# Optimization experiments

Hardware: AMD Instinct MI355X
Metric: run time of the kernel (lower is better)

The kernel has to match this reference:

```python
import jax, jax.numpy as jnp
import numpy as np

D_MODEL = 256
N_HEADS = 8
N_LEVELS = 4
N_POINTS = 4
D_FFN = 1024
DH = D_MODEL // N_HEADS
SPATIAL = [(100, 100), (50, 50), (25, 25), (13, 13)]  # (H_l, W_l) per level


def setup_inputs() -> dict:
    key = jax.random.key(0)
    ks = iter(jax.random.split(key, 40))
    N, Lq = 8, 900
    Lin = sum(h * w for h, w in SPATIAL)
    p = lambda shape: jax.random.normal(next(ks), shape, jnp.float32) * 0.02
    inp = {
        'idx': 0,
        'tgt': jax.random.normal(next(ks), (N, Lq, D_MODEL), jnp.float32),
        'query_pos': jax.random.normal(next(ks), (N, Lq, D_MODEL), jnp.float32),
        'reference_points_def': jax.random.uniform(next(ks), (N, Lq, N_LEVELS, 2), jnp.float32),
        'src': jax.random.normal(next(ks), (N, Lin, D_MODEL), jnp.float32),
        'src_spatial_shapes': jnp.array(SPATIAL, jnp.int32),
        'level_start_index': jnp.array(np.cumsum([0] + [h * w for h, w in SPATIAL])[:-1], jnp.int32),
        'src_padding_mask': jnp.zeros((N, Lin), bool),
        # self-attn params
        'wq': p((D_MODEL, D_MODEL)), 'bq': jnp.zeros((D_MODEL,)),
        'wk': p((D_MODEL, D_MODEL)), 'bk': jnp.zeros((D_MODEL,)),
        'wv': p((D_MODEL, D_MODEL)), 'bv': jnp.zeros((D_MODEL,)),
        'wo': p((D_MODEL, D_MODEL)), 'bo': jnp.zeros((D_MODEL,)),
        # MSDeformAttn params
        'w_val': p((D_MODEL, D_MODEL)), 'b_val': jnp.zeros((D_MODEL,)),
        'w_off': p((D_MODEL, N_HEADS * N_LEVELS * N_POINTS * 2)), 'b_off': p((N_HEADS * N_LEVELS * N_POINTS * 2,)),
        'w_att': p((D_MODEL, N_HEADS * N_LEVELS * N_POINTS)), 'b_att': jnp.zeros((N_HEADS * N_LEVELS * N_POINTS,)),
        'w_out': p((D_MODEL, D_MODEL)), 'b_out': jnp.zeros((D_MODEL,)),
        # layer norms
        'ln1_g': jnp.ones((D_MODEL,)), 'ln1_b': jnp.zeros((D_MODEL,)),
        'ln2_g': jnp.ones((D_MODEL,)), 'ln2_b': jnp.zeros((D_MODEL,)),
        'ln3_g': jnp.ones((D_MODEL,)), 'ln3_b': jnp.zeros((D_MODEL,)),
        # FFN
        'w1': p((D_MODEL, D_FFN)), 'b1': jnp.zeros((D_FFN,)),
        'w2': p((D_FFN, D_MODEL)), 'b2': jnp.zeros((D_MODEL,)),
    }
    return inp


def _ln(x, g, b):
    m = x.mean(-1, keepdims=True)
    v = jnp.var(x, axis=-1, keepdims=True)
    return (x - m) / jnp.sqrt(v + 1e-5) * g + b


def _mha(q, k, v, wq, bq, wk, bk, wv, bv, wo, bo):
    N, Lq, _ = q.shape
    split = lambda x: x.reshape(N, -1, N_HEADS, DH).transpose(0, 2, 1, 3)  # (N,H,L,dh)
    qh = split(q @ wq + bq) * (1.0 / np.sqrt(DH))
    kh = split(k @ wk + bk)
    vh = split(v @ wv + bv)
    attn = jax.nn.softmax(jnp.einsum('bhqd,bhkd->bhqk', qh, kh), axis=-1)
    o = jnp.einsum('bhqk,bhkd->bhqd', attn, vh).transpose(0, 2, 1, 3).reshape(N, Lq, D_MODEL)
    return o @ wo + bo


def _bilinear(vflat, Hl, Wl, loc):
    # vflat: (N, H, Hl*Wl, dh); loc: (N, Lq, H, P, 2) normalized (x, y) in [0,1]
    N, Lq, _, P, _ = loc.shape
    x = loc[..., 0] * Wl - 0.5  # align_corners=False pixel coords
    y = loc[..., 1] * Hl - 0.5
    x0 = jnp.floor(x); y0 = jnp.floor(y)
    fx = (x - x0).transpose(0, 2, 1, 3).reshape(N, N_HEADS, Lq * P, 1)
    fy = (y - y0).transpose(0, 2, 1, 3).reshape(N, N_HEADS, Lq * P, 1)
    x0i = x0.astype(jnp.int32); y0i = y0.astype(jnp.int32)

    def gather(xi, yi):
        valid = ((xi >= 0) & (xi < Wl) & (yi >= 0) & (yi < Hl)).astype(vflat.dtype)
        idx = jnp.clip(yi, 0, Hl - 1) * Wl + jnp.clip(xi, 0, Wl - 1)
        idx = idx.transpose(0, 2, 1, 3).reshape(N, N_HEADS, Lq * P)
        g = jnp.take_along_axis(vflat, idx[..., None], axis=2)  # (N,H,Lq*P,dh)
        return g * valid.transpose(0, 2, 1, 3).reshape(N, N_HEADS, Lq * P, 1)

    v = (gather(x0i, y0i) * (1 - fx) * (1 - fy)
         + gather(x0i + 1, y0i) * fx * (1 - fy)
         + gather(x0i, y0i + 1) * (1 - fx) * fy
         + gather(x0i + 1, y0i + 1) * fx * fy)
    return v.reshape(N, N_HEADS, Lq, P, DH)


def _msdeform(query, ref, src, ss, pad_mask, w_val, b_val, w_off, b_off, w_att, b_att, w_out, b_out):
    N, Lq, _ = query.shape
    value = src @ w_val + b_val
    value = jnp.where(pad_mask[..., None], 0.0, value)  # masked_fill on padded memory
    off = (query @ w_off + b_off).reshape(N, Lq, N_HEADS, N_LEVELS, N_POINTS, 2)
    att = jax.nn.softmax((query @ w_att + b_att).reshape(N, Lq, N_HEADS, N_LEVELS * N_POINTS), axis=-1)
    att = att.reshape(N, Lq, N_HEADS, N_LEVELS, N_POINTS)
    normalizer = jnp.array([[w, h] for h, w in ss], jnp.float32)  # (L, 2) as (W_l, H_l)
    loc = ref[:, :, None, :, None, :] + off / normalizer[None, None, None, :, None, :]
    out = jnp.zeros((N, N_HEADS, Lq, DH), value.dtype)
    start = 0
    for l, (Hl, Wl) in enumerate(ss):
        vflat = value[:, start:start + Hl * Wl].reshape(N, Hl * Wl, N_HEADS, DH).transpose(0, 2, 1, 3)
        samp = _bilinear(vflat, Hl, Wl, loc[:, :, :, l])  # (N,H,Lq,P,dh)
        w_l = att[:, :, :, l].transpose(0, 2, 1, 3)  # (N,H,Lq,P)
        out = out + (samp * w_l[..., None]).sum(3)
        start += Hl * Wl
    out = out.transpose(0, 2, 1, 3).reshape(N, Lq, D_MODEL)
    return out @ w_out + b_out, loc


def reference(idx, tgt, query_pos, reference_points_def, src, src_spatial_shapes, level_start_index,
              src_padding_mask, wq, bq, wk, bk, wv, bv, wo, bo,
              w_val, b_val, w_off, b_off, w_att, b_att, w_out, b_out,
              ln1_g, ln1_b, ln2_g, ln2_b, ln3_g, ln3_b, w1, b1, w2, b2):
    ss = [tuple(int(v) for v in row) for row in np.asarray(src_spatial_shapes)]
    # self-attention (is_contrastive=False path)
    q = tgt + query_pos
    tgt2 = _mha(q, q, tgt, wq, bq, wk, bk, wv, bv, wo, bo)
    tgt = _ln(tgt + tgt2, ln2_g, ln2_b)
    # multiscale deformable cross-attention
    tgt2, _ = _msdeform(tgt + query_pos, reference_points_def, src, ss, src_padding_mask,
                        w_val, b_val, w_off, b_off, w_att, b_att, w_out, b_out)
    tgt = _ln(tgt + tgt2, ln1_g, ln1_b)
    # FFN
    tgt2 = jax.nn.relu(tgt @ w1 + b1) @ w2 + b2
    tgt = _ln(tgt + tgt2, ln3_g, ln3_b)
    return tgt
```

## Files before the change

kernel.cpp:

```cpp
#include <hip/hip_runtime.h>
#include <math.h>

#define NB 8
#define LQ 900
#define DM 256
#define NH 8
#define DH 32
#define NL 4
#define NP 4
#define DFFN 1024
#define LIN 13294
#define NVAL (NB*LIN)
#define MROW (NB*LQ)

typedef __attribute__((ext_vector_type(8))) short bf16x8;
typedef __attribute__((ext_vector_type(4))) float f32x4;

__device__ __forceinline__ unsigned short f2bf(float x) {
  unsigned u = __float_as_uint(x);
  u += 0x7FFFu + ((u >> 16) & 1u);
  return (unsigned short)(u >> 16);
}

__global__ __launch_bounds__(256) void pack_w(const float* __restrict__ Win,
                                              unsigned short* __restrict__ Wp) {
  const int idx = blockIdx.x * 256 + threadIdx.x;
  const int e = idx & 7;
  const int cs = (idx >> 3) & 3;
  const int n = (idx >> 5) & 255;
  const int kt = idx >> 13;
  const int c = cs ^ ((n >> 1) & 3);
  const int k = kt * 32 + c * 8 + e;
  Wp[idx] = f2bf(Win[(size_t)k * 256 + n]);
}

__global__ __launch_bounds__(256) void value_gemm2(const float* __restrict__ A,
                                                   const unsigned short* __restrict__ Wp,
                                                   const float* __restrict__ bias,
                                                   unsigned short* __restrict__ C,
                                                   int M) {
  __shared__ char lds[17408];
  short* As = (short*)lds;
  short* Bs = (short*)(lds + 4096);
  const int tid = threadIdx.x;
  const int lane = tid & 63, w = tid >> 6;
  const int wr = w >> 1, wc = w & 1;
  const int l15 = lane & 15, lc = lane >> 4;
  const int nwg = gridDim.x;
  const int qq = nwg >> 3, rr = nwg & 7;
  const int xcd = blockIdx.x & 7, pos = blockIdx.x >> 3;
  const int wgid = (xcd < rr ? xcd * (qq + 1) : rr * (qq + 1) + (xcd - rr) * qq) + pos;
  const int m0 = (wgid >> 1) * 64, n0 = (wgid & 1) * 128;
  const int ar = tid >> 2, ac = tid & 3;
  f32x4 acc[2][4] = {};
  for (int kt = 0; kt < 8; kt++) {
    const int arow = min(m0 + ar, M - 1);
    const float* ap = A + (size_t)arow * 256 + kt * 32 + ac * 8;
    const float4 a0 = ((const float4*)ap)[0], a1 = ((const float4*)ap)[1];
    const unsigned short* bp = Wp + ((size_t)(kt * 256 + n0)) * 32 + tid * 16;
    const uint4 b0 = ((const uint4*)bp)[0], b1 = ((const uint4*)bp)[1];
    __syncthreads();
    {
      bf16x8 av;
      av[0] = (short)f2bf(a0.x); av[1] = (short)f2bf(a0.y);
      av[2] = (short)f2bf(a0.z); av[3] = (short)f2bf(a0.w);
      av[4] = (short)f2bf(a1.x); av[5] = (short)f2bf(a1.y);
      av[6] = (short)f2bf(a1.z); av[7] = (short)f2bf(a1.w);
      *(bf16x8*)&As[ar * 32 + ((ac ^ ((ar >> 1) & 3)) << 3)] = av;
      *(uint4*)&Bs[tid * 16] = b0;
      *(uint4*)&Bs[tid * 16 + 8] = b1;
    }
    __syncthreads();
    bf16x8 af[2], bq[4];
#pragma unroll
    for (int i = 0; i < 2; i++) {
      const int row = wr * 32 + i * 16 + l15;
      af[i] = *(const bf16x8*)&As[row * 32 + ((lc ^ ((row >> 1) & 3)) << 3)];
    }
#pragma unroll
    for (int q = 0; q < 4; q++) {
      const int col = wc * 64 + q * 16 + l15;
      bq[q] = *(const bf16x8*)&Bs[col * 32 + ((lc ^ ((col >> 1) & 3)) << 3)];
    }
#pragma unroll
    for (int i = 0; i < 2; i++)
#pragma unroll
      for (int q = 0; q < 4; q++)
        acc[i][q] = __builtin_amdgcn_mfma_f32_16x16x32_bf16(af[i], bq[q], acc[i][q], 0, 0, 0);
  }
  __syncthreads();
  short* strip = (short*)lds + w * 2176;
  float bv[4];
#pragma unroll
  for (int q = 0; q < 4; q++) bv[q] = bias[n0 + wc * 64 + q * 16 + l15];
#pragma unroll
  for (int i = 0; i < 2; i++)
#pragma unroll
    for (int q = 0; q < 4; q++)
#pragma unroll
      for (int r = 0; r < 4; r++)
        strip[(i * 16 + lc * 4 + r) * 68 + q * 16 + l15] = (short)f2bf(acc[i][q][r] + bv[q]);
  __syncthreads();
#pragma unroll
  for (int p = 0; p < 4; p++) {
    const int row = p * 8 + (lane >> 3), c8 = lane & 7;
    const bf16x8 v = *(const bf16x8*)&strip[row * 68 + c8 * 8];
    const int grow = m0 + wr * 32 + row;
    if (grow < M)
      *(bf16x8*)(C + (size_t)grow * 256 + n0 + wc * 64 + c8 * 8) = v;
  }
}

#define LDSW 40
__device__ __forceinline__ void gemm_body(const void* Aptr, const float* A2,
                                          const float* __restrict__ W,
                                          const float* __restrict__ bias, void* Cptr,
                                          int M, int Nn, int K, float scale, int relu,
                                          int a_bf16, int out_bf16, int m0, int n0,
                                          short* As, short* Bs) {
  const int tid = threadIdx.x;
  const int lane = tid & 63, w = tid >> 6;
  const int wr = w >> 1, wc = w & 1;
  const int ar = tid >> 2, ac = (tid & 3) << 3;
  const int bk = tid >> 3, bn = (tid & 7) << 3;
  const int aswz = (((ac >> 3) ^ (ar >> 3)) & 3) << 3;
  const int l15 = lane & 15, lc = lane >> 4;
  const int arow = min(m0 + ar, M - 1);
  f32x4 acc[2][2] = {};
  for (int kt = 0; kt < K; kt += 32) {
    bf16x8 av;
    if (a_bf16) {
      av = *(const bf16x8*)((const unsigned short*)Aptr + (size_t)arow * K + kt + ac);
    } else {
      const float* ap = (const float*)Aptr + (size_t)arow * K + kt + ac;
      float4 a0 = ((const float4*)ap)[0], a1 = ((const float4*)ap)[1];
      if (A2) {
        const float* a2p = A2 + (size_t)arow * K + kt + ac;
        const float4 c0 = ((const float4*)a2p)[0], c1 = ((const float4*)a2p)[1];
        a0.x += c0.x; a0.y += c0.y; a0.z += c0.z; a0.w += c0.w;
        a1.x += c1.x; a1.y += c1.y; a1.z += c1.z; a1.w += c1.w;
      }
      av[0] = (short)f2bf(a0.x); av[1] = (short)f2bf(a0.y);
      av[2] = (short)f2bf(a0.z); av[3] = (short)f2bf(a0.w);
      av[4] = (short)f2bf(a1.x); av[5] = (short)f2bf(a1.y);
      av[6] = (short)f2bf(a1.z); av[7] = (short)f2bf(a1.w);
    }
    const float* wp = W + (size_t)(kt + bk) * Nn + n0 + bn;
    const float4 b0 = ((const float4*)wp)[0], b1 = ((const float4*)wp)[1];
    __syncthreads();
    {
      *(bf16x8*)&As[ar * LDSW + aswz] = av;
      unsigned short bb[8] = {f2bf(b0.x), f2bf(b0.y), f2bf(b0.z), f2bf(b0.w),
                              f2bf(b1.x), f2bf(b1.y), f2bf(b1.z), f2bf(b1.w)};
      const int bchunk = bk >> 3, bke = bk & 7;
#pragma unroll
      for (int j = 0; j < 8; j++) {
        const int n = bn + j;
        Bs[n * LDSW + (((bchunk ^ (n >> 3)) & 3) << 3) + bke] = (short)bb[j];
      }
    }
    __syncthreads();
    bf16x8 af[2], bf[2];
#pragma unroll
    for (int i = 0; i < 2; i++) {
      const int row = wr * 32 + i * 16 + l15;
      af[i] = *(const bf16x8*)&As[row * LDSW + (((lc ^ (row >> 3)) & 3) << 3)];
      const int col = wc * 32 + i * 16 + l15;
      bf[i] = *(const bf16x8*)&Bs[col * LDSW + (((lc ^ (col >> 3)) & 3) << 3)];
    }
#pragma unroll
    for (int i = 0; i < 2; i++)
#pragma unroll
      for (int j = 0; j < 2; j++)
        acc[i][j] = __builtin_amdgcn_mfma_f32_16x16x32_bf16(af[i], bf[j], acc[i][j], 0, 0, 0);
  }
#pragma unroll
  for (int i = 0; i < 2; i++) {
    const int row0 = m0 + wr * 32 + i * 16 + lc * 4;
#pragma unroll
    for (int j = 0; j < 2; j++) {
      const int col = n0 + wc * 32 + j * 16 + l15;
      const float bv = bias[col];
#pragma unroll
      for (int r = 0; r < 4; r++) {
        const int row = row0 + r;
        if (row < M) {
          float v = (acc[i][j][r] + bv) * scale;
          if (relu) v = fmaxf(v, 0.f);
          if (out_bf16)
            ((unsigned short*)Cptr)[(size_t)row * Nn + col] = f2bf(v);
          else
            ((float*)Cptr)[(size_t)row * Nn + col] = v;
        }
      }
    }
  }
}

__global__ __launch_bounds__(256) void gemm_qkv(const float* __restrict__ tgt,
                                                const float* __restrict__ qpos,
                                                const float* __restrict__ wq, const float* __restrict__ bq_,
                                                const float* __restrict__ wk, const float* __restrict__ bk_,
                                                const float* __restrict__ wv, const float* __restrict__ bv_,
                                                unsigned short* Qb, unsigned short* Kb, unsigned short* Vb,
                                                float qscale) {
  __shared__ short As[64 * LDSW];
  __shared__ short Bs[64 * LDSW];
  const int z = blockIdx.z;
  const float* W = (z == 0) ? wq : (z == 1) ? wk : wv;
  const float* bias = (z == 0) ? bq_ : (z == 1) ? bk_ : bv_;
  unsigned short* C = (z == 0) ? Qb : (z == 1) ? Kb : Vb;
  const float* A2 = (z == 2) ? nullptr : qpos;
  gemm_body(tgt, A2, W, bias, C, MROW, DM, DM, (z == 0) ? qscale : 1.f, 0, 0, 1,
            blockIdx.y * 64, blockIdx.x * 64, As, Bs);
}

__global__ __launch_bounds__(256) void gemm_offatt(const float* __restrict__ x1,
                                                   const float* __restrict__ qpos,
                                                   const float* __restrict__ w_off, const float* __restrict__ b_off,
                                                   const float* __restrict__ w_att, const float* __restrict__ b_att,
                                                   float* offb, float* attb) {
  const int z = blockIdx.z;
  if (z == 1 && blockIdx.x >= 2) return;
  __shared__ short As[64 * LDSW];
  __shared__ short Bs[64 * LDSW];
  const float* W = z ? w_att : w_off;
  const float* bias = z ? b_att : b_off;
  float* C = z ? attb : offb;
  const int Nn = z ? 128 : 256;
  gemm_body(x1, qpos, W, bias, C, MROW, Nn, DM, 1.f, 0, 0, 0,
            blockIdx.y * 64, blockIdx.x * 64, As, Bs);
}

__global__ __launch_bounds__(256) void gemm_fused(const void* A, const float* W, const float* bias,
                                                  void* C, int M, int Nn, int K, float scale,
                                                  int relu, int a_bf16, int out_bf16) {
  __shared__ short As[64 * LDSW];
  __shared__ short Bs[64 * LDSW];
  gemm_body(A, nullptr, W, bias, C, M, Nn, K, scale, relu, a_bf16, out_bf16,
            blockIdx.y * 64, blockIdx.x * 64, As, Bs);
}

__global__ __launch_bounds__(256) void attn_mfma(const unsigned short* __restrict__ Qg,
                                                 const unsigned short* __restrict__ Kg,
                                                 const unsigned short* __restrict__ Vg,
                                                 float* __restrict__ O) {
  __shared__ short Ks[2048];
  __shared__ short Vt[2048];
  __shared__ short Pl[4096];
  const int tid = threadIdx.x;
  const int lane = tid & 63, w = tid >> 6;
  const int l15 = lane & 15, lc = lane >> 4;
  const int h = blockIdx.y, b = blockIdx.z;
  const int q0 = blockIdx.x * 64;
  char* KsB = (char*)Ks; char* VtB = (char*)Vt; char* PlB = (char*)Pl + w * 2048;

  bf16x8 qa;
  {
    const int qrow = min(q0 + w * 16 + l15, LQ - 1);
    qa = *(const bf16x8*)(Qg + ((size_t)(b * LQ + qrow)) * DM + h * DH + lc * 8);
  }
  f32x4 o0 = {0.f, 0.f, 0.f, 0.f}, o1 = {0.f, 0.f, 0.f, 0.f};
  float mrow[4], lrow[4];
#pragma unroll
  for (int r = 0; r < 4; r++) { mrow[r] = -1e30f; lrow[r] = 0.f; }
  const int skey = tid >> 2, sq = tid & 3;

  for (int kt = 0; kt < LQ; kt += 64) {
    const int kr = min(kt + skey, LQ - 1);
    const bf16x8 kb = *(const bf16x8*)(Kg + ((size_t)(b * LQ + kr)) * DM + h * DH + sq * 8);
    const bf16x8 vv = *(const bf16x8*)(Vg + ((size_t)(b * LQ + kr)) * DM + h * DH + sq * 8);
    __syncthreads();
    {
      *(bf16x8*)(KsB + ((skey * 64 + sq * 16) ^ ((skey & 7) << 4))) = kb;
#pragma unroll
      for (int j = 0; j < 8; j++) {
        const int dh = sq * 8 + j;
        const int qz = ((dh & 7) ^ (((dh >> 3) & 3) << 1)) << 4;
        *(short*)(VtB + ((dh * 128 + skey * 2) ^ qz)) = (short)vv[j];
      }
    }
    __syncthreads();
    f32x4 s[4];
#pragma unroll
    for (int cb = 0; cb < 4; cb++) {
      const int key = cb * 16 + l15;
      const bf16x8 kf = *(const bf16x8*)(KsB + ((key * 64 + lc * 16) ^ ((key & 7) << 4)));
      const f32x4 z = {0.f, 0.f, 0.f, 0.f};
      s[cb] = __builtin_amdgcn_mfma_f32_16x16x32_bf16(qa, kf, z, 0, 0, 0);
    }
#pragma unroll
    for (int cb = 0; cb < 4; cb++)
      if (kt + cb * 16 + l15 >= LQ) {
        s[cb][0] = -1e30f; s[cb][1] = -1e30f; s[cb][2] = -1e30f; s[cb][3] = -1e30f;
      }
    float tm[4], fs[4], ps[4];
#pragma unroll
    for (int r = 0; r < 4; r++)
      tm[r] = fmaxf(fmaxf(s[0][r], s[1][r]), fmaxf(s[2][r], s[3][r]));
#pragma unroll
    for (int msk = 1; msk <= 8; msk <<= 1)
#pragma unroll
      for (int r = 0; r < 4; r++) tm[r] = fmaxf(tm[r], __shfl_xor(tm[r], msk));
#pragma unroll
    for (int r = 0; r < 4; r++) {
      const float nm = fmaxf(mrow[r], tm[r]);
      fs[r] = __expf(mrow[r] - nm);
      mrow[r] = nm;
    }
#pragma unroll
    for (int cb = 0; cb < 4; cb++)
#pragma unroll
      for (int r = 0; r < 4; r++) s[cb][r] = __expf(s[cb][r] - mrow[r]);
#pragma unroll
    for (int r = 0; r < 4; r++) ps[r] = (s[0][r] + s[1][r]) + (s[2][r] + s[3][r]);
#pragma unroll
    for (int msk = 1; msk <= 8; msk <<= 1)
#pragma unroll
      for (int r = 0; r < 4; r++) ps[r] += __shfl_xor(ps[r], msk);
#pragma unroll
    for (int r = 0; r < 4; r++) {
      lrow[r] = lrow[r] * fs[r] + ps[r];
      o0[r] *= fs[r]; o1[r] *= fs[r];
    }
#pragma unroll
    for (int cb = 0; cb < 4; cb++)
#pragma unroll
      for (int r = 0; r < 4; r++) {
        const int row = lc * 4 + r, col = cb * 16 + l15;
        *(short*)(PlB + ((row * 128 + col * 2) ^ ((row & 7) << 4))) = (short)f2bf(s[cb][r]);
      }
#pragma unroll
    for (int ks2 = 0; ks2 < 2; ks2++) {
      const int koff2 = (ks2 * 32 + lc * 8) * 2;
      const bf16x8 pa = *(const bf16x8*)(PlB + ((l15 * 128 + koff2) ^ ((l15 & 7) << 4)));
      {
        const int dh = l15;
        const int qz = ((dh & 7) ^ (((dh >> 3) & 3) << 1)) << 4;
        const bf16x8 vf = *(const bf16x8*)(VtB + ((dh * 128 + koff2) ^ qz));
        o0 = __builtin_amdgcn_mfma_f32_16x16x32_bf16(pa, vf, o0, 0, 0, 0);
      }
      {
        const int dh = 16 + l15;
        const int qz = ((dh & 7) ^ (((dh >> 3) & 3) << 1)) << 4;
        const bf16x8 vf = *(const bf16x8*)(VtB + ((dh * 128 + koff2) ^ qz));
        o1 = __builtin_amdgcn_mfma_f32_16x16x32_bf16(pa, vf, o1, 0, 0, 0);
      }
    }
  }
#pragma unroll
  for (int r = 0; r < 4; r++) {
    const int qrow = q0 + w * 16 + lc * 4 + r;
    if (qrow < LQ) {
      const float inv = 1.f / lrow[r];
      float* op = O + ((size_t)(b * LQ + qrow)) * DM + h * DH;
      op[l15] = o0[r] * inv;
      op[16 + l15] = o1[r] * inv;
    }
  }
}

__global__ __launch_bounds__(256) void sample_kernel(const unsigned short* __restrict__ value,
                                                     const float* __restrict__ ref,
                                                     const float* __restrict__ off,
                                                     const float* __restrict__ att,
                                                     float* __restrict__ out) {
  const int t = blockIdx.x * 256 + threadIdx.x;
  const int d8 = t & 3;
  const int h = (t >> 2) & 7;
  const int qb = t >> 5;
  const int b = qb / LQ;
  const int HLs[4] = {100, 50, 25, 13};
  const int STs[4] = {0, 10000, 12500, 13125};
  const float* rp = ref + (size_t)qb * (NL * 2);
  const float* op = off + (size_t)qb * DM + h * (NL * NP * 2);
  const float* ap = att + (size_t)qb * (NH * NL * NP) + h * (NL * NP);
  const unsigned short* vb = value + (size_t)b * LIN * DM + h * DH + d8 * 8;

  float aw[16];
#pragma unroll
  for (int i = 0; i < 4; i++) {
    const float4 a4 = ((const float4*)ap)[i];
    aw[4 * i] = a4.x; aw[4 * i + 1] = a4.y; aw[4 * i + 2] = a4.z; aw[4 * i + 3] = a4.w;
  }
  float am = aw[0];
#pragma unroll
  for (int i = 1; i < 16; i++) am = fmaxf(am, aw[i]);
  float asum = 0.f;
#pragma unroll
  for (int i = 0; i < 16; i++) { aw[i] = __expf(aw[i] - am); asum += aw[i]; }
  const float ainv = 1.f / asum;

  float acc[8] = {};
#pragma unroll
  for (int l = 0; l < NL; l++) {
    const int Hl = HLs[l], Wl = HLs[l], st = STs[l];
    const float rx = rp[l * 2], ry = rp[l * 2 + 1];
#pragma unroll
    for (int p = 0; p < NP; p++) {
      const float2 o2 = ((const float2*)op)[l * NP + p];
      const float a = aw[l * NP + p] * ainv;
      const float locx = rx + o2.x / (float)Wl;
      const float locy = ry + o2.y / (float)Hl;
      const float x = locx * (float)Wl - 0.5f;
      const float y = locy * (float)Hl - 0.5f;
      const float xf = floorf(x), yf = floorf(y);
      const float fx = x - xf, fy = y - yf;
      const int x0 = (int)xf, y0 = (int)yf;
      const int x1 = x0 + 1, y1 = y0 + 1;
      const float vx0 = (x0 >= 0 && x0 < Wl) ? 1.f : 0.f;
      const float vx1 = (x1 >= 0 && x1 < Wl) ? 1.f : 0.f;
      const float vy0 = (y0 >= 0 && y0 < Hl) ? 1.f : 0.f;
      const float vy1 = (y1 >= 0 && y1 < Hl) ? 1.f : 0.f;
      const int cx0 = min(max(x0, 0), Wl - 1), cx1 = min(max(x1, 0), Wl - 1);
      const int cy0 = min(max(y0, 0), Hl - 1), cy1 = min(max(y1, 0), Hl - 1);
      const float w00 = a * (1.f - fx) * (1.f - fy) * vx0 * vy0;
      const float w10 = a * fx * (1.f - fy) * vx1 * vy0;
      const float w01 = a * (1.f - fx) * fy * vx0 * vy1;
      const float w11 = a * fx * fy * vx1 * vy1;
      const unsigned short* r0 = vb + (size_t)(st + cy0 * Wl) * DM;
      const unsigned short* r1 = vb + (size_t)(st + cy1 * Wl) * DM;
      const uint4 g00 = *(const uint4*)(r0 + (size_t)cx0 * DM);
      const uint4 g10 = *(const uint4*)(r0 + (size_t)cx1 * DM);
      const uint4 g01 = *(const uint4*)(r1 + (size_t)cx0 * DM);
      const uint4 g11 = *(const uint4*)(r1 + (size_t)cx1 * DM);
      const unsigned u00[4] = {g00.x, g00.y, g00.z, g00.w};
      const unsigned u10[4] = {g10.x, g10.y, g10.z, g10.w};
      const unsigned u01[4] = {g01.x, g01.y, g01.z, g01.w};
      const unsigned u11[4] = {g11.x, g11.y, g11.z, g11.w};
#pragma unroll
      for (int i = 0; i < 4; i++) {
        acc[2 * i]     += w00 * __uint_as_float(u00[i] << 16) + w10 * __uint_as_float(u10[i] << 16)
                        + w01 * __uint_as_float(u01[i] << 16) + w11 * __uint_as_float(u11[i] << 16);
        acc[2 * i + 1] += w00 * __uint_as_float(u00[i] & 0xFFFF0000u) + w10 * __uint_as_float(u10[i] & 0xFFFF0000u)
                        + w01 * __uint_as_float(u01[i] & 0xFFFF0000u) + w11 * __uint_as_float(u11[i] & 0xFFFF0000u);
      }
    }
  }
  float* o = out + (size_t)t * 8;
  *(float4*)o = make_float4(acc[0], acc[1], acc[2], acc[3]);
  *(float4*)(o + 4) = make_float4(acc[4], acc[5], acc[6], acc[7]);
}

__global__ __launch_bounds__(64) void ln_kernel(const float* __restrict__ A,
                                                const float* __restrict__ R,
                                                const float* __restrict__ g,
                                                const float* __restrict__ be,
                                                float* __restrict__ out) {
  const int row = blockIdx.x, t = threadIdx.x;
  const float4 va = ((const float4*)(A + (size_t)row * DM))[t];
  const float4 vr = ((const float4*)(R + (size_t)row * DM))[t];
  const float x0 = va.x + vr.x, x1 = va.y + vr.y, x2 = va.z + vr.z, x3 = va.w + vr.w;
  float s = x0 + x1 + x2 + x3;
  float ss = x0 * x0 + x1 * x1 + x2 * x2 + x3 * x3;
#pragma unroll
  for (int o = 1; o < 64; o <<= 1) { s += __shfl_xor(s, o); ss += __shfl_xor(ss, o); }
  const float mean = s * (1.f / DM);
  const float var = ss * (1.f / DM) - mean * mean;
  const float rstd = rsqrtf(var + 1e-5f);
  const float4 vg = ((const float4*)g)[t];
  const float4 vb = ((const float4*)be)[t];
  float4 o4;
  o4.x = (x0 - mean) * rstd * vg.x + vb.x;
  o4.y = (x1 - mean) * rstd * vg.y + vb.y;
  o4.z = (x2 - mean) * rstd * vg.z + vb.z;
  o4.w = (x3 - mean) * rstd * vg.w + vb.w;
  ((float4*)(out + (size_t)row * DM))[t] = o4;
}

extern "C" void kernel_launch(void* const* d_in, const int* in_sizes, int n_in,
                              void* d_out, int out_size, void* d_ws, size_t ws_size,
                              hipStream_t stream) {
  const float* tgt  = (const float*)d_in[1];
  const float* qpos = (const float*)d_in[2];
  const float* ref  = (const float*)d_in[3];
  const float* src  = (const float*)d_in[4];
  const float* wq = (const float*)d_in[8];  const float* bq = (const float*)d_in[9];
  const float* wk = (const float*)d_in[10]; const float* bk = (const float*)d_in[11];
  const float* wv = (const float*)d_in[12]; const float* bv = (const float*)d_in[13];
  const float* wo = (const float*)d_in[14]; const float* bo = (const float*)d_in[15];
  const float* w_val = (const float*)d_in[16]; const float* b_val = (const float*)d_in[17];
  const float* w_off = (const float*)d_in[18]; const float* b_off = (const float*)d_in[19];
  const float* w_att = (const float*)d_in[20]; const float* b_att = (const float*)d_in[21];
  const float* w_out = (const float*)d_in[22]; const float* b_out = (const float*)d_in[23];
  const float* ln1g = (const float*)d_in[24]; const float* ln1b = (const float*)d_in[25];
  const float* ln2g = (const float*)d_in[26]; const float* ln2b = (const float*)d_in[27];
  const float* ln3g = (const float*)d_in[28]; const float* ln3b = (const float*)d_in[29];
  const float* w1 = (const float*)d_in[30]; const float* b1 = (const float*)d_in[31];
  const float* w2 = (const float*)d_in[32]; const float* b2 = (const float*)d_in[33];

  const size_t S = (size_t)MROW * DM;
  const size_t VAL_F = (size_t)NVAL * DM;
  float* ws = (float*)d_ws;
  float* value = ws;
  unsigned short* wp = (unsigned short*)(ws + VAL_F / 2);
  float* B0   = ws + VAL_F;
  unsigned short* Qb = (unsigned short*)(B0 + 1 * S);
  unsigned short* Kb = (unsigned short*)(B0 + 2 * S);
  unsigned short* Vb = (unsigned short*)(B0 + 3 * S);
  float* Ob   = B0 + 4 * S;
  float* tmp  = B0 + 5 * S;
  float* x1   = B0 + 0 * S;
  float* offb = B0 + 2 * S;
  float* attb = B0 + 3 * S;
  float* samp = B0 + 4 * S;
  float* x2   = B0 + 6 * S;
  unsigned short* hffn = (unsigned short*)(B0 + 1 * S);

  const float qscale = 0.17677669529663687f;
  const dim3 blk(256);
  const dim3 gQ(DM / 64, (MROW + 63) / 64);
  const int gVal2 = 2 * ((NVAL + 63) / 64);

  gemm_qkv<<<dim3(4, 113, 3), blk, 0, stream>>>(tgt, qpos, wq, bq, wk, bk, wv, bv,
                                                Qb, Kb, Vb, qscale);
  attn_mfma<<<dim3((LQ + 63) / 64, NH, NB), blk, 0, stream>>>(Qb, Kb, Vb, Ob);
  gemm_fused<<<gQ, blk, 0, stream>>>(Ob, wo, bo, tmp, MROW, DM, DM, 1.f, 0, 0, 0);
  ln_kernel<<<dim3(MROW), dim3(64), 0, stream>>>(tmp, tgt, ln2g, ln2b, x1);

  pack_w<<<dim3(256), blk, 0, stream>>>(w_val, wp);
  value_gemm2<<<dim3(gVal2), blk, 0, stream>>>(src, wp, b_val, (unsigned short*)value, NVAL);
  gemm_offatt<<<dim3(4, 113, 2), blk, 0, stream>>>(x1, qpos, w_off, b_off, w_att, b_att,
                                                   offb, attb);
  sample_kernel<<<dim3((MROW * NH * 4) / 256), blk, 0, stream>>>(
      (const unsigned short*)value, ref, offb, attb, samp);
  gemm_fused<<<gQ, blk, 0, stream>>>(samp, w_out, b_out, tmp, MROW, DM, DM, 1.f, 0, 0, 0);
  ln_kernel<<<dim3(MROW), dim3(64), 0, stream>>>(tmp, x1, ln1g, ln1b, x2);

  gemm_fused<<<dim3(DFFN / 64, 113), blk, 0, stream>>>(x2, w1, b1, hffn, MROW, DFFN, DM,
                                                       1.f, 1, 0, 1);
  gemm_fused<<<gQ, blk, 0, stream>>>(hffn, w2, b2, tmp, MROW, DM, DFFN, 1.f, 0, 1, 0);
  ln_kernel<<<dim3(MROW), dim3(64), 0, stream>>>(tmp, x2, ln3g, ln3b, (float*)d_out);
}
```

Measured before the change: 257.2 us.

## Merge value projection with QKV GEMM into one launch; emit bf16 intermediates

The value-projection GEMM and the Q/K/V projection GEMM are combined into a single kernel launch whose block index picks either the value tile or a QKV tile. This lets the two independent GEMMs share the GPU at once instead of running back to back with low occupancy in between. Separately, the attention output and the deformable sampling output are now stored as bf16, and the following output-projection GEMMs read bf16 inputs. This halves their write and read traffic at the cost of earlier rounding.

```diff
diff --git a/kernel.cpp b/kernel.cpp
--- a/kernel.cpp
+++ b/kernel.cpp
@@ -12,6 +12,8 @@
 #define LIN 13294
 #define NVAL (NB*LIN)
 #define MROW (NB*LQ)
+#define GVAL2 3324
+#define GQKV 1356
 
 typedef __attribute__((ext_vector_type(8))) short bf16x8;
 typedef __attribute__((ext_vector_type(4))) float f32x4;
@@ -34,21 +36,19 @@
   Wp[idx] = f2bf(Win[(size_t)k * 256 + n]);
 }
 
-__global__ __launch_bounds__(256) void value_gemm2(const float* __restrict__ A,
-                                                   const unsigned short* __restrict__ Wp,
-                                                   const float* __restrict__ bias,
-                                                   unsigned short* __restrict__ C,
-                                                   int M) {
-  __shared__ char lds[17408];
+__device__ __forceinline__ void value_body(const float* __restrict__ A,
+                                           const unsigned short* __restrict__ Wp,
+                                           const float* __restrict__ bias,
+                                           unsigned short* __restrict__ C,
+                                           int M, char* lds, int bidx, int nwg) {
   short* As = (short*)lds;
   short* Bs = (short*)(lds + 4096);
   const int tid = threadIdx.x;
   const int lane = tid & 63, w = tid >> 6;
   const int wr = w >> 1, wc = w & 1;
   const int l15 = lane & 15, lc = lane >> 4;
-  const int nwg = gridDim.x;
   const int qq = nwg >> 3, rr = nwg & 7;
-  const int xcd = blockIdx.x & 7, pos = blockIdx.x >> 3;
+  const int xcd = bidx & 7, pos = bidx >> 3;
   const int wgid = (xcd < rr ? xcd * (qq + 1) : rr * (qq + 1) + (xcd - rr) * qq) + pos;
   const int m0 = (wgid >> 1) * 64, n0 = (wgid & 1) * 128;
   const int ar = tid >> 2, ac = tid & 3;
@@ -197,22 +197,30 @@
   }
 }
 
-__global__ __launch_bounds__(256) void gemm_qkv(const float* __restrict__ tgt,
-                                                const float* __restrict__ qpos,
-                                                const float* __restrict__ wq, const float* __restrict__ bq_,
-                                                const float* __restrict__ wk, const float* __restrict__ bk_,
-                                                const float* __restrict__ wv, const float* __restrict__ bv_,
-                                                unsigned short* Qb, unsigned short* Kb, unsigned short* Vb,
-                                                float qscale) {
-  __shared__ short As[64 * LDSW];
-  __shared__ short Bs[64 * LDSW];
-  const int z = blockIdx.z;
-  const float* W = (z == 0) ? wq : (z == 1) ? wk : wv;
-  const float* bias = (z == 0) ? bq_ : (z == 1) ? bk_ : bv_;
-  unsigned short* C = (z == 0) ? Qb : (z == 1) ? Kb : Vb;
-  const float* A2 = (z == 2) ? nullptr : qpos;
-  gemm_body(tgt, A2, W, bias, C, MROW, DM, DM, (z == 0) ? qscale : 1.f, 0, 0, 1,
-            blockIdx.y * 64, blockIdx.x * 64, As, Bs);
+__global__ __launch_bounds__(256) void stage1_kernel(
+    const float* __restrict__ src, const unsigned short* __restrict__ Wp,
+    const float* __restrict__ b_val, unsigned short* Vout,
+    const float* __restrict__ tgt, const float* __restrict__ qpos,
+    const float* __restrict__ wq, const float* __restrict__ bq_,
+    const float* __restrict__ wk, const float* __restrict__ bk_,
+    const float* __restrict__ wv, const float* __restrict__ bv_,
+    unsigned short* Qb, unsigned short* Kb, unsigned short* Vb, float qscale) {
+  __shared__ char lds[17408];
+  if (blockIdx.x < GVAL2) {
+    value_body(src, Wp, b_val, Vout, NVAL, lds, blockIdx.x, GVAL2);
+  } else {
+    const int bid = blockIdx.x - GVAL2;
+    const int z = bid / 452, rem = bid - z * 452;
+    const int nx = rem & 3, my = rem >> 2;
+    short* As = (short*)lds;
+    short* Bs = (short*)(lds + 64 * LDSW * 2);
+    const float* W = (z == 0) ? wq : (z == 1) ? wk : wv;
+    const float* bias = (z == 0) ? bq_ : (z == 1) ? bk_ : bv_;
+    unsigned short* C = (z == 0) ? Qb : (z == 1) ? Kb : Vb;
+    const float* A2 = (z == 2) ? nullptr : qpos;
+    gemm_body(tgt, A2, W, bias, C, MROW, DM, DM, (z == 0) ? qscale : 1.f, 0, 0, 1,
+              my * 64, nx * 64, As, Bs);
+  }
 }
 
 __global__ __launch_bounds__(256) void gemm_offatt(const float* __restrict__ x1,
@@ -244,7 +252,7 @@
 __global__ __launch_bounds__(256) void attn_mfma(const unsigned short* __restrict__ Qg,
                                                  const unsigned short* __restrict__ Kg,
                                                  const unsigned short* __restrict__ Vg,
-                                                 float* __restrict__ O) {
+                                                 unsigned short* __restrict__ O) {
   __shared__ short Ks[2048];
   __shared__ short Vt[2048];
   __shared__ short Pl[4096];
@@ -353,9 +361,9 @@
     const int qrow = q0 + w * 16 + lc * 4 + r;
     if (qrow < LQ) {
       const float inv = 1.f / lrow[r];
-      float* op = O + ((size_t)(b * LQ + qrow)) * DM + h * DH;
-      op[l15] = o0[r] * inv;
-      op[16 + l15] = o1[r] * inv;
+      unsigned short* op = O + ((size_t)(b * LQ + qrow)) * DM + h * DH;
+      op[l15] = f2bf(o0[r] * inv);
+      op[16 + l15] = f2bf(o1[r] * inv);
     }
   }
 }
@@ -364,7 +372,7 @@
                                                      const float* __restrict__ ref,
                                                      const float* __restrict__ off,
                                                      const float* __restrict__ att,
-                                                     float* __restrict__ out) {
+                                                     unsigned short* __restrict__ out) {
   const int t = blockIdx.x * 256 + threadIdx.x;
   const int d8 = t & 3;
   const int h = (t >> 2) & 7;
@@ -437,9 +445,10 @@
       }
     }
   }
-  float* o = out + (size_t)t * 8;
-  *(float4*)o = make_float4(acc[0], acc[1], acc[2], acc[3]);
-  *(float4*)(o + 4) = make_float4(acc[4], acc[5], acc[6], acc[7]);
+  bf16x8 ov;
+#pragma unroll
+  for (int i = 0; i < 8; i++) ov[i] = (short)f2bf(acc[i]);
+  *(bf16x8*)(out + (size_t)t * 8) = ov;
 }
 
 __global__ __launch_bounds__(64) void ln_kernel(const float* __restrict__ A,
@@ -498,33 +507,33 @@
   unsigned short* Qb = (unsigned short*)(B0 + 1 * S);
   unsigned short* Kb = (unsigned short*)(B0 + 2 * S);
   unsigned short* Vb = (unsigned short*)(B0 + 3 * S);
-  float* Ob   = B0 + 4 * S;
+  unsigned short* Ob = (unsigned short*)(B0 + 4 * S);
   float* tmp  = B0 + 5 * S;
   float* x1   = B0 + 0 * S;
   float* offb = B0 + 2 * S;
   float* attb = B0 + 3 * S;
-  float* samp = B0 + 4 * S;
+  unsigned short* samp = (unsigned short*)(B0 + 4 * S);
   float* x2   = B0 + 6 * S;
   unsigned short* hffn = (unsigned short*)(B0 + 1 * S);
 
   const float qscale = 0.17677669529663687f;
   const dim3 blk(256);
   const dim3 gQ(DM / 64, (MROW + 63) / 64);
-  const int gVal2 = 2 * ((NVAL + 63) / 64);
-
-  gemm_qkv<<<dim3(4, 113, 3), blk, 0, stream>>>(tgt, qpos, wq, bq, wk, bk, wv, bv,
-                                                Qb, Kb, Vb, qscale);
+
+  pack_w<<<dim3(256), blk, 0, stream>>>(w_val, wp);
+  stage1_kernel<<<dim3(GVAL2 + GQKV), blk, 0, stream>>>(
+      src, wp, b_val, (unsigned short*)value, tgt, qpos,
+      wq, bq, wk, bk, wv, bv, Qb, Kb, Vb, qscale);
+
   attn_mfma<<<dim3((LQ + 63) / 64, NH, NB), blk, 0, stream>>>(Qb, Kb, Vb, Ob);
-  gemm_fused<<<gQ, blk, 0, stream>>>(Ob, wo, bo, tmp, MROW, DM, DM, 1.f, 0, 0, 0);
+  gemm_fused<<<gQ, blk, 0, stream>>>(Ob, wo, bo, tmp, MROW, DM, DM, 1.f, 0, 1, 0);
   ln_kernel<<<dim3(MROW), dim3(64), 0, stream>>>(tmp, tgt, ln2g, ln2b, x1);
 
-  pack_w<<<dim3(256), blk, 0, stream>>>(w_val, wp);
-  value_gemm2<<<dim3(gVal2), blk, 0, stream>>>(src, wp, b_val, (unsigned short*)value, NVAL);
   gemm_offatt<<<dim3(4, 113, 2), blk, 0, stream>>>(x1, qpos, w_off, b_off, w_att, b_att,
                                                    offb, attb);
   sample_kernel<<<dim3((MROW * NH * 4) / 256), blk, 0, stream>>>(
       (const unsigned short*)value, ref, offb, attb, samp);
-  gemm_fused<<<gQ, blk, 0, stream>>>(samp, w_out, b_out, tmp, MROW, DM, DM, 1.f, 0, 0, 0);
+  gemm_fused<<<gQ, blk, 0, stream>>>(samp, w_out, b_out, tmp, MROW, DM, DM, 1.f, 0, 1, 0);
   ln_kernel<<<dim3(MROW), dim3(64), 0, stream>>>(tmp, x1, ln1g, ln1b, x2);
 
   gemm_fused<<<dim3(DFFN / 64, 113), blk, 0, stream>>>(x2, w1, b1, hffn, MROW, DFFN, DM,
```

Measured after the change: 269.2 us. 1.05x slower.

## Prepack all weights to swizzled bf16 and emit bf16 attention/sampling outputs

Applied to the files above, without the earlier changes.

All weight matrices are converted once per call into a pre-swizzled bf16 layout by a single pack kernel. The generic GEMM then loads B tiles with one 16-byte copy per thread instead of converting fp32 and scattering element-wise into LDS. The attention and deformable-sampling kernels now write bf16 outputs, which halves the traffic into the output projections. LayerNorm runs four rows per 256-thread block. This adds a pack kernel covering about 1M weights and lowers the precision of intermediate activations.

```diff
diff --git a/kernel.cpp b/kernel.cpp
--- a/kernel.cpp
+++ b/kernel.cpp
@@ -12,6 +12,19 @@
 #define LIN 13294
 #define NVAL (NB*LIN)
 #define MROW (NB*LQ)
+#define GVAL2 3324
+
+#define WP_VAL 0
+#define WP_Q   65536
+#define WP_K   131072
+#define WP_V   196608
+#define WP_O   262144
+#define WP_OFF 327680
+#define WP_ATT 393216
+#define WP_OUT 425984
+#define WP_W1  491520
+#define WP_W2  753664
+#define WP_TOT 1015808
 
 typedef __attribute__((ext_vector_type(8))) short bf16x8;
 typedef __attribute__((ext_vector_type(4))) float f32x4;
@@ -22,16 +35,32 @@
   return (unsigned short)(u >> 16);
 }
 
-__global__ __launch_bounds__(256) void pack_w(const float* __restrict__ Win,
-                                              unsigned short* __restrict__ Wp) {
+__global__ __launch_bounds__(256) void pack_all(
+    const float* __restrict__ w_val, const float* __restrict__ wq,
+    const float* __restrict__ wk, const float* __restrict__ wv,
+    const float* __restrict__ wo, const float* __restrict__ w_off,
+    const float* __restrict__ w_att, const float* __restrict__ w_out,
+    const float* __restrict__ w1, const float* __restrict__ w2,
+    unsigned short* __restrict__ Wp) {
   const int idx = blockIdx.x * 256 + threadIdx.x;
-  const int e = idx & 7;
-  const int cs = (idx >> 3) & 3;
-  const int n = (idx >> 5) & 255;
-  const int kt = idx >> 13;
+  const float* src; int r, logN;
+  if (idx < WP_Q)        { src = w_val; r = idx;          logN = 8; }
+  else if (idx < WP_K)   { src = wq;    r = idx - WP_Q;   logN = 8; }
+  else if (idx < WP_V)   { src = wk;    r = idx - WP_K;   logN = 8; }
+  else if (idx < WP_O)   { src = wv;    r = idx - WP_V;   logN = 8; }
+  else if (idx < WP_OFF) { src = wo;    r = idx - WP_O;   logN = 8; }
+  else if (idx < WP_ATT) { src = w_off; r = idx - WP_OFF; logN = 8; }
+  else if (idx < WP_OUT) { src = w_att; r = idx - WP_ATT; logN = 7; }
+  else if (idx < WP_W1)  { src = w_out; r = idx - WP_OUT; logN = 8; }
+  else if (idx < WP_W2)  { src = w1;    r = idx - WP_W1;  logN = 10; }
+  else                   { src = w2;    r = idx - WP_W2;  logN = 8; }
+  const int N = 1 << logN;
+  const int e = r & 7, cs = (r >> 3) & 3;
+  const int n = (r >> 5) & (N - 1);
+  const int kt = r >> (5 + logN);
   const int c = cs ^ ((n >> 1) & 3);
   const int k = kt * 32 + c * 8 + e;
-  Wp[idx] = f2bf(Win[(size_t)k * 256 + n]);
+  Wp[idx] = f2bf(src[(size_t)k * N + n]);
 }
 
 __global__ __launch_bounds__(256) void value_gemm2(const float* __restrict__ A,
@@ -111,9 +140,8 @@
   }
 }
 
-#define LDSW 40
 __device__ __forceinline__ void gemm_body(const void* Aptr, const float* A2,
-                                          const float* __restrict__ W,
+                                          const unsigned short* __restrict__ Wp,
                                           const float* __restrict__ bias, void* Cptr,
                                           int M, int Nn, int K, float scale, int relu,
                                           int a_bf16, int out_bf16, int m0, int n0,
@@ -121,21 +149,19 @@
   const int tid = threadIdx.x;
   const int lane = tid & 63, w = tid >> 6;
   const int wr = w >> 1, wc = w & 1;
-  const int ar = tid >> 2, ac = (tid & 3) << 3;
-  const int bk = tid >> 3, bn = (tid & 7) << 3;
-  const int aswz = (((ac >> 3) ^ (ar >> 3)) & 3) << 3;
+  const int ar = tid >> 2, ac = tid & 3;
   const int l15 = lane & 15, lc = lane >> 4;
   const int arow = min(m0 + ar, M - 1);
   f32x4 acc[2][2] = {};
   for (int kt = 0; kt < K; kt += 32) {
     bf16x8 av;
     if (a_bf16) {
-      av = *(const bf16x8*)((const unsigned short*)Aptr + (size_t)arow * K + kt + ac);
+      av = *(const bf16x8*)((const unsigned short*)Aptr + (size_t)arow * K + kt + ac * 8);
     } else {
-      const float* ap = (const float*)Aptr + (size_t)arow * K + kt + ac;
+      const float* ap = (const float*)Aptr + (size_t)arow * K + kt + ac * 8;
       float4 a0 = ((const float4*)ap)[0], a1 = ((const float4*)ap)[1];
       if (A2) {
-        const float* a2p = A2 + (size_t)arow * K + kt + ac;
+        const float* a2p = A2 + (size_t)arow * K + kt + ac * 8;
         const float4 c0 = ((const float4*)a2p)[0], c1 = ((const float4*)a2p)[1];
         a0.x += c0.x; a0.y += c0.y; a0.z += c0.z; a0.w += c0.w;
         a1.x += c1.x; a1.y += c1.y; a1.z += c1.z; a1.w += c1.w;
@@ -145,28 +171,19 @@
       av[4] = (short)f2bf(a1.x); av[5] = (short)f2bf(a1.y);
       av[6] = (short)f2bf(a1.z); av[7] = (short)f2bf(a1.w);
     }
-    const float* wp = W + (size_t)(kt + bk) * Nn + n0 + bn;
-    const float4 b0 = ((const float4*)wp)[0], b1 = ((const float4*)wp)[1];
+    const unsigned short* bp = Wp + ((size_t)((kt >> 5) * Nn + n0)) * 32 + tid * 8;
+    const uint4 b0 = *(const uint4*)bp;
     __syncthreads();
-    {
-      *(bf16x8*)&As[ar * LDSW + aswz] = av;
-      unsigned short bb[8] = {f2bf(b0.x), f2bf(b0.y), f2bf(b0.z), f2bf(b0.w),
-                              f2bf(b1.x), f2bf(b1.y), f2bf(b1.z), f2bf(b1.w)};
-      const int bchunk = bk >> 3, bke = bk & 7;
-#pragma unroll
-      for (int j = 0; j < 8; j++) {
-        const int n = bn + j;
-        Bs[n * LDSW + (((bchunk ^ (n >> 3)) & 3) << 3) + bke] = (short)bb[j];
-      }
-    }
+    *(bf16x8*)&As[ar * 32 + ((ac ^ ((ar >> 1) & 3)) << 3)] = av;
+    *(uint4*)&Bs[tid * 8] = b0;
     __syncthreads();
     bf16x8 af[2], bf[2];
 #pragma unroll
     for (int i = 0; i < 2; i++) {
       const int row = wr * 32 + i * 16 + l15;
-      af[i] = *(const bf16x8*)&As[row * LDSW + (((lc ^ (row >> 3)) & 3) << 3)];
+      af[i] = *(const bf16x8*)&As[row * 32 + ((lc ^ ((row >> 1) & 3)) << 3)];
       const int col = wc * 32 + i * 16 + l15;
-      bf[i] = *(const bf16x8*)&Bs[col * LDSW + (((lc ^ (col >> 3)) & 3) << 3)];
+      bf[i] = *(const bf16x8*)&Bs[col * 32 + ((lc ^ ((col >> 1) & 3)) << 3)];
     }
 #pragma unroll
     for (int i = 0; i < 2; i++)
@@ -199,15 +216,16 @@
 
 __global__ __launch_bounds__(256) void gemm_qkv(const float* __restrict__ tgt,
                                                 const float* __restrict__ qpos,
-                                                const float* __restrict__ wq, const float* __restrict__ bq_,
-                                                const float* __restrict__ wk, const float* __restrict__ bk_,
-                                                const float* __restrict__ wv, const float* __restrict__ bv_,
-                                                unsigned short* Qb, unsigned short* Kb, unsigned short* Vb,
-                                                float qscale) {
-  __shared__ short As[64 * LDSW];
-  __shared__ short Bs[64 * LDSW];
+                                                const unsigned short* __restrict__ Wp,
+                                                const float* __restrict__ bq_,
+                                                const float* __restrict__ bk_,
+                                                const float* __restrict__ bv_,
+                                                unsigned short* Qb, unsigned short* Kb,
+                                                unsigned short* Vb, float qscale) {
+  __shared__ short As[64 * 32];
+  __shared__ short Bs[64 * 32];
   const int z = blockIdx.z;
-  const float* W = (z == 0) ? wq : (z == 1) ? wk : wv;
+  const unsigned short* W = Wp + (z == 0 ? WP_Q : z == 1 ? WP_K : WP_V);
   const float* bias = (z == 0) ? bq_ : (z == 1) ? bk_ : bv_;
   unsigned short* C = (z == 0) ? Qb : (z == 1) ? Kb : Vb;
   const float* A2 = (z == 2) ? nullptr : qpos;
@@ -217,14 +235,15 @@
 
 __global__ __launch_bounds__(256) void gemm_offatt(const float* __restrict__ x1,
                                                    const float* __restrict__ qpos,
-                                                   const float* __restrict__ w_off, const float* __restrict__ b_off,
-                                                   const float* __restrict__ w_att, const float* __restrict__ b_att,
+                                                   const unsigned short* __restrict__ Wp,
+                                                   const float* __restrict__ b_off,
+                                                   const float* __restrict__ b_att,
                                                    float* offb, float* attb) {
   const int z = blockIdx.z;
   if (z == 1 && blockIdx.x >= 2) return;
-  __shared__ short As[64 * LDSW];
-  __shared__ short Bs[64 * LDSW];
-  const float* W = z ? w_att : w_off;
+  __shared__ short As[64 * 32];
+  __shared__ short Bs[64 * 32];
+  const unsigned short* W = Wp + (z ? WP_ATT : WP_OFF);
   const float* bias = z ? b_att : b_off;
   float* C = z ? attb : offb;
   const int Nn = z ? 128 : 256;
@@ -232,19 +251,20 @@
             blockIdx.y * 64, blockIdx.x * 64, As, Bs);
 }
 
-__global__ __launch_bounds__(256) void gemm_fused(const void* A, const float* W, const float* bias,
-                                                  void* C, int M, int Nn, int K, float scale,
-                                                  int relu, int a_bf16, int out_bf16) {
-  __shared__ short As[64 * LDSW];
-  __shared__ short Bs[64 * LDSW];
-  gemm_body(A, nullptr, W, bias, C, M, Nn, K, scale, relu, a_bf16, out_bf16,
+__global__ __launch_bounds__(256) void gemm_fused(const void* A, const unsigned short* Wp,
+                                                  const float* bias, void* C, int M, int Nn,
+                                                  int K, float scale, int relu, int a_bf16,
+                                                  int out_bf16) {
+  __shared__ short As[64 * 32];
+  __shared__ short Bs[64 * 32];
+  gemm_body(A, nullptr, Wp, bias, C, M, Nn, K, scale, relu, a_bf16, out_bf16,
             blockIdx.y * 64, blockIdx.x * 64, As, Bs);
 }
 
 __global__ __launch_bounds__(256) void attn_mfma(const unsigned short* __restrict__ Qg,
                                                  const unsigned short* __restrict__ Kg,
                                                  const unsigned short* __restrict__ Vg,
-                                                 float* __restrict__ O) {
+                                                 unsigned short* __restrict__ O) {
   __shared__ short Ks[2048];
   __shared__ short Vt[2048];
   __shared__ short Pl[4096];
@@ -353,9 +373,9 @@
     const int qrow = q0 + w * 16 + lc * 4 + r;
     if (qrow < LQ) {
       const float inv = 1.f / lrow[r];
-      float* op = O + ((size_t)(b * LQ + qrow)) * DM + h * DH;
-      op[l15] = o0[r] * inv;
-      op[16 + l15] = o1[r] * inv;
+      unsigned short* op = O + ((size_t)(b * LQ + qrow)) * DM + h * DH;
+      op[l15] = f2bf(o0[r] * inv);
+      op[16 + l15] = f2bf(o1[r] * inv);
     }
   }
 }
@@ -364,7 +384,7 @@
                                                      const float* __restrict__ ref,
                                                      const float* __restrict__ off,
                                                      const float* __restrict__ att,
-                                                     float* __restrict__ out) {
+                                                     unsigned short* __restrict__ out) {
   const int t = blockIdx.x * 256 + threadIdx.x;
   const int d8 = t & 3;
   const int h = (t >> 2) & 7;
@@ -437,17 +457,19 @@
       }
     }
   }
-  float* o = out + (size_t)t * 8;
-  *(float4*)o = make_float4(acc[0], acc[1], acc[2], acc[3]);
-  *(float4*)(o + 4) = make_float4(acc[4], acc[5], acc[6], acc[7]);
-}
-
-__global__ __launch_bounds__(64) void ln_kernel(const float* __restrict__ A,
-                                                const float* __restrict__ R,
-                                                const float* __restrict__ g,
-                                                const float* __restrict__ be,
-                                                float* __restrict__ out) {
-  const int row = blockIdx.x, t = threadIdx.x;
+  bf16x8 ov;
+#pragma unroll
+  for (int i = 0; i < 8; i++) ov[i] = (short)f2bf(acc[i]);
+  *(bf16x8*)(out + (size_t)t * 8) = ov;
+}
+
+__global__ __launch_bounds__(256) void ln_kernel(const float* __restrict__ A,
+                                                 const float* __restrict__ R,
+                                                 const float* __restrict__ g,
+                                                 const float* __restrict__ be,
+                                                 float* __restrict__ out) {
+  const int row = blockIdx.x * 4 + (threadIdx.x >> 6);
+  const int t = threadIdx.x & 63;
   const float4 va = ((const float4*)(A + (size_t)row * DM))[t];
   const float4 vr = ((const float4*)(R + (size_t)row * DM))[t];
   const float x0 = va.x + vr.x, x1 = va.y + vr.y, x2 = va.z + vr.z, x3 = va.w + vr.w;
@@ -498,37 +520,40 @@
   unsigned short* Qb = (unsigned short*)(B0 + 1 * S);
   unsigned short* Kb = (unsigned short*)(B0 + 2 * S);
   unsigned short* Vb = (unsigned short*)(B0 + 3 * S);
-  float* Ob   = B0 + 4 * S;
+  unsigned short* Ob = (unsigned short*)(B0 + 4 * S);
   float* tmp  = B0 + 5 * S;
   float* x1   = B0 + 0 * S;
   float* offb = B0 + 2 * S;
   float* attb = B0 + 3 * S;
-  float* samp = B0 + 4 * S;
+  unsigned short* samp = (unsigned short*)(B0 + 4 * S);
   float* x2   = B0 + 6 * S;
   unsigned short* hffn = (unsigned short*)(B0 + 1 * S);
 
   const float qscale = 0.17677669529663687f;
   const dim3 blk(256);
   const dim3 gQ(DM / 64, (MROW + 63) / 64);
-  const int gVal2 = 2 * ((NVAL + 63) / 64);
-
-  gemm_qkv<<<dim3(4, 113, 3), blk, 0, stream>>>(tgt, qpos, wq, bq, wk, bk, wv, bv,
+
+  pack_all<<<dim3(WP_TOT / 256), blk, 0, stream>>>(w_val, wq, wk, wv, wo, w_off, w_att,
+                                                   w_out, w1, w2, wp);
+
+  gemm_qkv<<<dim3(4, 113, 3), blk, 0, stream>>>(tgt, qpos, wp, bq, bk, bv,
                                                 Qb, Kb, Vb, qscale);
   attn_mfma<<<dim3((LQ + 63) / 64, NH, NB), blk, 0, stream>>>(Qb, Kb, Vb, Ob);
-  gemm_fused<<<gQ, blk, 0, stream>>>(Ob, wo, bo, tmp, MROW, DM, DM, 1.f, 0, 0, 0);
-  ln_kernel<<<dim3(MROW), dim3(64), 0, stream>>>(tmp, tgt, ln2g, ln2b, x1);
-
-  pack_w<<<dim3(256), blk, 0, stream>>>(w_val, wp);
-  value_gemm2<<<dim3(gVal2), blk, 0, stream>>>(src, wp, b_val, (unsigned short*)value, NVAL);
-  gemm_offatt<<<dim3(4, 113, 2), blk, 0, stream>>>(x1, qpos, w_off, b_off, w_att, b_att,
-                                                   offb, attb);
+  gemm_fused<<<gQ, blk, 0, stream>>>(Ob, wp + WP_O, bo, tmp, MROW, DM, DM, 1.f, 0, 1, 0);
+  ln_kernel<<<dim3(MROW / 4), blk, 0, stream>>>(tmp, tgt, ln2g, ln2b, x1);
+
+  value_gemm2<<<dim3(GVAL2), blk, 0, stream>>>(src, wp + WP_VAL, b_val,
+                                               (unsigned short*)value, NVAL);
+  gemm_offatt<<<dim3(4, 113, 2), blk, 0, stream>>>(x1, qpos, wp, b_off, b_att, offb, attb);
   sample_kernel<<<dim3((MROW * NH * 4) / 256), blk, 0, stream>>>(
       (const unsigned short*)value, ref, offb, attb, samp);
-  gemm_fused<<<gQ, blk, 0, stream>>>(samp, w_out, b_out, tmp, MROW, DM, DM, 1.f, 0, 0, 0);
-  ln_kernel<<<dim3(MROW), dim3(64), 0, stream>>>(tmp, x1, ln1g, ln1b, x2);
-
-  gemm_fused<<<dim3(DFFN / 64, 113), blk, 0, stream>>>(x2, w1, b1, hffn, MROW, DFFN, DM,
-                                                       1.f, 1, 0, 1);
-  gemm_fused<<<gQ, blk, 0, stream>>>(hffn, w2, b2, tmp, MROW, DM, DFFN, 1.f, 0, 1, 0);
-  ln_kernel<<<dim3(MROW), dim3(64), 0, stream>>>(tmp, x2, ln3g, ln3b, (float*)d_out);
-}
+  gemm_fused<<<gQ, blk, 0, stream>>>(samp, wp + WP_OUT, b_out, tmp, MROW, DM, DM,
+                                     1.f, 0, 1, 0);
+  ln_kernel<<<dim3(MROW / 4), blk, 0, stream>>>(tmp, x1, ln1g, ln1b, x2);
+
+  gemm_fused<<<dim3(DFFN / 64, 113), blk, 0, stream>>>(x2, wp + WP_W1, b1, hffn, MROW,
+                                                       DFFN, DM, 1.f, 1, 0, 1);
+  gemm_fused<<<gQ, blk, 0, stream>>>(hffn, wp + WP_W2, b2, tmp, MROW, DM, DFFN,
+                                     1.f, 0, 1, 0);
+  ln_kernel<<<dim3(MROW / 4), blk, 0, stream>>>(tmp, x2, ln3g, ln3b, (float*)d_out);
+}
```

Measured after the change: 256.8 us. No clear change (-0.2%).
